# Performance work log

Hardware: AMD Instinct MI355X
Metric: run time of the kernel (lower is better)

Reference implementation:

```python
import math
import jax, jax.numpy as jnp
import numpy as np

B, L, D = 2, 2048, 2048
H, DH = 16, 128
DFF = 8192


def setup_inputs() -> dict:
    key = jax.random.key(0)
    ks = jax.random.split(key, 9)
    x = jax.random.normal(ks[0], (B, L, D), dtype=jnp.float32)
    # additive causal mask: 0 on/below diagonal, -inf above
    neg = jnp.finfo(jnp.float32).min
    mask = jnp.where(jnp.tril(jnp.ones((L, L), dtype=bool)), 0.0, neg)[None, None]
    s = 0.02
    return {
        "x": x,
        "mask": mask,
        "ln1_w": jnp.ones((D,), jnp.float32),
        "wq": jax.random.normal(ks[1], (D, D), jnp.float32) * s,
        "wk": jax.random.normal(ks[2], (D, D), jnp.float32) * s,
        "wv": jax.random.normal(ks[3], (D, D), jnp.float32) * s,
        "wo": jax.random.normal(ks[4], (D, D), jnp.float32) * s,
        "ln2_w": jnp.ones((D,), jnp.float32),
        "w_up": jax.random.normal(ks[5], (DFF, D), jnp.float32) * s,
        "w_down": jax.random.normal(ks[6], (D, DFF), jnp.float32) * s,
    }


def _rmsnorm(x, w, eps=1e-8):
    rms = jnp.sqrt(jnp.mean(x * x, axis=-1, keepdims=True) + eps)
    return x / rms * w


def reference(x, mask, ln1_w, wq, wk, wv, wo, ln2_w, w_up, w_down):
    h = _rmsnorm(x, ln1_w)
    # torch Linear: y = x @ W.T ; weights are [out, in]
    q = (h @ wq.T).reshape(B, L, H, DH).transpose(0, 2, 1, 3)  # [B,H,L,DH]
    k = (h @ wk.T).reshape(B, L, H, DH).transpose(0, 2, 1, 3)
    v = (h @ wv.T).reshape(B, L, H, DH).transpose(0, 2, 1, 3)
    scores = jnp.einsum('bhqd,bhkd->bhqk', q, k) / math.sqrt(DH)
    scores = scores + mask
    attn = jax.nn.softmax(scores, axis=-1)
    out = jnp.einsum('bhqk,bhkd->bhqd', attn, v)
    out = out.transpose(0, 2, 1, 3).reshape(B, L, D)
    x = x + out @ wo.T
    h = _rmsnorm(x, ln2_w)
    ff = jax.nn.gelu(h @ w_up.T, approximate=False) @ w_down.T  # exact erf GELU as in F.gelu
    return x + ff
```

## Files before the change

### kernel.cpp

```cpp
#include <hip/hip_runtime.h>
#include <hip/hip_bf16.h>
#include <math.h>

#define B_   2
#define L_   2048
#define D_   2048
#define H_   16
#define DH_  128
#define DFF_ 8192
#define NTOK (B_*L_)

typedef __attribute__((ext_vector_type(8))) short bf16x8;
typedef __attribute__((ext_vector_type(4))) float floatx4;
typedef unsigned short u16;

__device__ __forceinline__ u16 f2bf(float f) {
    union { float f; unsigned u; } c; c.f = f;
    unsigned r = (c.u + 0x7fffu + ((c.u >> 16) & 1u)) >> 16;
    return (u16)r;
}

__device__ __forceinline__ void async_cp16(const u16* g, u16* l) {
    __builtin_amdgcn_global_load_lds(
        (const __attribute__((address_space(1))) unsigned int*)g,
        (__attribute__((address_space(3))) unsigned int*)l,
        16, 0, 0);
}

__global__ __launch_bounds__(256) void cvt_bf16(const float* __restrict__ in,
                                                u16* __restrict__ out, int n4) {
    int i = blockIdx.x * 256 + threadIdx.x;
    if (i >= n4) return;
    float4 v = ((const float4*)in)[i];
    ushort4 o = { f2bf(v.x), f2bf(v.y), f2bf(v.z), f2bf(v.w) };
    ((ushort4*)out)[i] = o;
}

__global__ __launch_bounds__(256) void rmsnorm_kernel(const float* __restrict__ x,
                                                      const float* __restrict__ w,
                                                      u16* __restrict__ out) {
    const int row = blockIdx.x, tid = threadIdx.x;
    const float* xr = x + (size_t)row * D_;
    float4 a = ((const float4*)xr)[tid];
    float4 b = ((const float4*)xr)[tid + 256];
    float ss = a.x*a.x + a.y*a.y + a.z*a.z + a.w*a.w
             + b.x*b.x + b.y*b.y + b.z*b.z + b.w*b.w;
#pragma unroll
    for (int d = 1; d < 64; d <<= 1) ss += __shfl_xor(ss, d, 64);
    __shared__ float sred[4];
    if ((tid & 63) == 0) sred[tid >> 6] = ss;
    __syncthreads();
    float tot = sred[0] + sred[1] + sred[2] + sred[3];
    float inv = 1.0f / sqrtf(tot * (1.0f / D_) + 1e-8f);
    float4 w0 = ((const float4*)w)[tid];
    float4 w1 = ((const float4*)w)[tid + 256];
    ushort4 o0 = { f2bf(a.x*inv*w0.x), f2bf(a.y*inv*w0.y), f2bf(a.z*inv*w0.z), f2bf(a.w*inv*w0.w) };
    ushort4 o1 = { f2bf(b.x*inv*w1.x), f2bf(b.y*inv*w1.y), f2bf(b.z*inv*w1.z), f2bf(b.w*inv*w1.w) };
    ushort4* orow = (ushort4*)(out + (size_t)row * D_);
    orow[tid] = o0;
    orow[tid + 256] = o1;
}


template<int MODE>
__global__ __launch_bounds__(512, 2) void gemm256(const u16* __restrict__ A,
                                                  const u16* __restrict__ Bw,
                                                  void* __restrict__ outp,
                                                  void* __restrict__ outp2,
                                                  const float* __restrict__ residual,
                                                  int M, int N, int K, float scale) {
    __shared__ __attribute__((aligned(16))) u16 lds_a[2][256 * 64];
    __shared__ __attribute__((aligned(16))) u16 lds_b[2][256 * 64];
    const int tid = threadIdx.x;
    const int wave = tid >> 6, lane = tid & 63;
    const int qd = lane >> 4, c16 = lane & 15;
    const int wm = wave >> 2, wn = wave & 3;
    const int gx = gridDim.x;
    const int nwg = gx * gridDim.y;
    const int orig = blockIdx.y * gx + blockIdx.x;
    const int id2 = (orig & 7) * (nwg >> 3) + (orig >> 3);
    const long tile_m = (long)(id2 / gx) * 256, tile_n = (long)(id2 % gx) * 256;
    const int NT = K >> 6;

    const int srow = tid >> 3;
    const int scol = (((tid & 7) ^ (srow & 7))) * 8;
    const u16* Asrc = A + (tile_m + srow) * (long)K + scol;
    const u16* Bsrc = Bw + (tile_n + srow) * (long)K + scol;
    const int stoff = tid * 8;

#define STAGE_A2(bi, g0, g1, ko) do { \
        async_cp16(Asrc + (long)(g0) * 64 * K + (ko), &lds_a[bi][(g0) * 4096 + stoff]); \
        async_cp16(Asrc + (long)(g1) * 64 * K + (ko), &lds_a[bi][(g1) * 4096 + stoff]); \
    } while (0)
#define STAGE_B2(bi, g0, g1, ko) do { \
        async_cp16(Bsrc + (long)(g0) * 64 * K + (ko), &lds_b[bi][(g0) * 4096 + stoff]); \
        async_cp16(Bsrc + (long)(g1) * 64 * K + (ko), &lds_b[bi][(g1) * 4096 + stoff]); \
    } while (0)

    const int csw = (qd * 16) ^ ((c16 & 7) << 4);
    const int arowb = (wm * 128 + c16) * 128;
    const int browb = (wn * 64 + c16) * 128;
#define LDAF(bi, i, ks) (*(const bf16x8*)((const char*)&lds_a[bi][0] + arowb + (i) * 2048 + (csw ^ ((ks) * 64))))
#define LDBF(bi, j, ks) (*(const bf16x8*)((const char*)&lds_b[bi][0] + browb + (j) * 2048 + (csw ^ ((ks) * 64))))
#define MFMA_(a, b, c) __builtin_amdgcn_mfma_f32_16x16x32_bf16(a, b, c, 0, 0, 0)

#define READ_BFR(bi) do { \
        _Pragma("unroll") \
        for (int j = 0; j < 4; j++) { bfr[j][0] = LDBF(bi, j, 0); bfr[j][1] = LDBF(bi, j, 1); } \
    } while (0)
#define READ_AF(dst, bi, r0) do { \
        dst[0] = LDAF(bi, r0, 0); dst[1] = LDAF(bi, r0, 1); \
        dst[2] = LDAF(bi, (r0) + 1, 0); dst[3] = LDAF(bi, (r0) + 1, 1); \
    } while (0)
#define MFMA_PH(af, R) do { \
        __builtin_amdgcn_s_setprio(1); \
        _Pragma("unroll") \
        for (int j = 0; j < 4; j++) acc[R][j]       = MFMA_(af[0], bfr[j][0], acc[R][j]); \
        _Pragma("unroll") \
        for (int j = 0; j < 4; j++) acc[(R) + 1][j] = MFMA_(af[2], bfr[j][0], acc[(R) + 1][j]); \
        _Pragma("unroll") \
        for (int j = 0; j < 4; j++) acc[R][j]       = MFMA_(af[1], bfr[j][1], acc[R][j]); \
        _Pragma("unroll") \
        for (int j = 0; j < 4; j++) acc[(R) + 1][j] = MFMA_(af[3], bfr[j][1], acc[(R) + 1][j]); \
        __builtin_amdgcn_s_setprio(0); \
    } while (0)

    floatx4 acc[8][4] = {};
    bf16x8 bfr[4][2];

    STAGE_B2(0, 0, 1, 0); STAGE_B2(0, 2, 3, 0);
    STAGE_A2(0, 0, 2, 0); STAGE_A2(0, 1, 3, 0);
    STAGE_B2(1, 0, 1, 64); STAGE_B2(1, 2, 3, 64);
    STAGE_A2(1, 0, 2, 64);
    asm volatile("s_waitcnt vmcnt(6)" ::: "memory");
    __builtin_amdgcn_s_barrier();

#define TILE256(bi, koN, koNN, GA1, GS) do { \
        READ_BFR(bi); \
        bf16x8 afA[4], afB[4]; \
        READ_AF(afA, bi, 0); \
         \
        READ_AF(afB, bi, 2); \
        if (GA1) STAGE_A2((bi) ^ 1, 1, 3, koN); \
        MFMA_PH(afA, 0); \
        __builtin_amdgcn_s_barrier(); \
         \
        READ_AF(afA, bi, 4); \
        if (GS) STAGE_B2(bi, 0, 1, koNN); \
        MFMA_PH(afB, 2); \
        __builtin_amdgcn_s_barrier(); \
         \
        READ_AF(afB, bi, 6); \
        if (GS) STAGE_B2(bi, 2, 3, koNN); \
        MFMA_PH(afA, 4); \
        __builtin_amdgcn_s_barrier(); \
         \
        if (GS) STAGE_A2(bi, 0, 2, koNN); \
        MFMA_PH(afB, 6); \
        if (GS) asm volatile("s_waitcnt vmcnt(6)" ::: "memory"); \
        else    asm volatile("s_waitcnt vmcnt(0)" ::: "memory"); \
        __builtin_amdgcn_s_barrier(); \
    } while (0)

    for (int t = 0; t < NT; t += 2) {
        const int s2 = (t + 2) < NT;
        const long ko1 = (long)(t + 1) * 64;
        const long ko2 = (long)(t + 2) * 64;
        const long ko3 = (long)(t + 3) * 64;
        TILE256(0, ko1, ko2, 1, s2);
        TILE256(1, ko2, ko3, s2, s2);
    }

#pragma unroll
    for (int i = 0; i < 8; i++) {
#pragma unroll
        for (int j = 0; j < 4; j++) {
#pragma unroll
            for (int r = 0; r < 4; r++) {
                long m = tile_m + wm * 128 + i * 16 + qd * 4 + r;
                long n = tile_n + wn * 64 + j * 16 + c16;
                float v = acc[i][j][r];
                if (MODE == 0) {
                    long b = m >> 11, l = m & 2047;
                    int isq = n < D_;
                    long f = n & 2047, h = f >> 7, dh = f & 127;
                    u16* dst = isq ? (u16*)outp : (u16*)outp2;
                    dst[((b * H_ + h) * (long)L_ + l) * DH_ + dh] =
                        f2bf(v * (isq ? scale : 1.0f));
                } else if (MODE == 1) {
                    long idx = m * (long)N + n;
                    ((float*)outp)[idx] = v + residual[idx];
                } else if (MODE == 2) {
                    float g = 0.5f * v * (1.0f + erff(v * 0.70710678118654752f));
                    ((u16*)outp)[m * (long)N + n] = f2bf(g);
                } else {
                    ((u16*)outp)[m * (long)N + n] = f2bf(v);
                }
            }
        }
    }
#undef TILE256
#undef READ_BFR
#undef READ_AF
#undef MFMA_PH
#undef STAGE_A2
#undef STAGE_B2
#undef LDAF
#undef LDBF
#undef MFMA_
}

template<int MODE>
__global__ __launch_bounds__(512, 2) void gemm128n(const u16* __restrict__ A,
                                                   const u16* __restrict__ Bw,
                                                   void* __restrict__ outp,
                                                   const float* __restrict__ residual,
                                                   int M, int N, int K) {
    __shared__ __attribute__((aligned(16))) u16 lds_a[2][128 * 64];
    __shared__ __attribute__((aligned(16))) u16 lds_b[2][256 * 64];
    const int tid = threadIdx.x;
    const int wave = tid >> 6, lane = tid & 63;
    const int qd = lane >> 4, c16 = lane & 15;
    const int wm = wave >> 2, wn = wave & 3;
    const int gx = gridDim.x;
    const int nwg = gx * gridDim.y;
    const int orig = blockIdx.y * gx + blockIdx.x;
    const int id2 = (orig & 7) * (nwg >> 3) + (orig >> 3);
    const long tile_m = (long)(id2 / gx) * 128, tile_n = (long)(id2 % gx) * 256;
    const int NT = K >> 6;

    const int srow = tid >> 3;
    const int scol = (((tid & 7) ^ (srow & 7))) * 8;
    const u16* Asrc = A + (tile_m + srow) * (long)K + scol;
    const u16* Bsrc = Bw + (tile_n + srow) * (long)K + scol;
    const int stoff = tid * 8;

#define STAGE_AA(bi, ko) do { \
        async_cp16(Asrc + (ko), &lds_a[bi][stoff]); \
        async_cp16(Asrc + 64 * (long)K + (ko), &lds_a[bi][4096 + stoff]); \
    } while (0)
#define STAGE_BA(bi, ko) do { \
        async_cp16(Bsrc + (ko), &lds_b[bi][stoff]); \
        async_cp16(Bsrc + 64 * (long)K + (ko), &lds_b[bi][4096 + stoff]); \
        async_cp16(Bsrc + 128 * (long)K + (ko), &lds_b[bi][8192 + stoff]); \
        async_cp16(Bsrc + 192 * (long)K + (ko), &lds_b[bi][12288 + stoff]); \
    } while (0)

    const int csw = (qd * 16) ^ ((c16 & 7) << 4);
    const int arowb = (wm * 64 + c16) * 128;
    const int browb = (wn * 64 + c16) * 128;
#define LDAF2(bi, i, ks) (*(const bf16x8*)((const char*)&lds_a[bi][0] + arowb + (i) * 2048 + (csw ^ ((ks) * 64))))
#define LDBF2(bi, j, ks) (*(const bf16x8*)((const char*)&lds_b[bi][0] + browb + (j) * 2048 + (csw ^ ((ks) * 64))))
#define MFMA_(a, b, c) __builtin_amdgcn_mfma_f32_16x16x32_bf16(a, b, c, 0, 0, 0)

#define READ_BFR2(bi) do { \
        _Pragma("unroll") \
        for (int j = 0; j < 4; j++) { bfr[j][0] = LDBF2(bi, j, 0); bfr[j][1] = LDBF2(bi, j, 1); } \
    } while (0)
#define READ_AF2(dst, bi, r0) do { \
        dst[0] = LDAF2(bi, r0, 0); dst[1] = LDAF2(bi, r0, 1); \
        dst[2] = LDAF2(bi, (r0) + 1, 0); dst[3] = LDAF2(bi, (r0) + 1, 1); \
    } while (0)
#define MFMA_PH2(af, R) do { \
        __builtin_amdgcn_s_setprio(1); \
        _Pragma("unroll") \
        for (int j = 0; j < 4; j++) acc[R][j]       = MFMA_(af[0], bfr[j][0], acc[R][j]); \
        _Pragma("unroll") \
        for (int j = 0; j < 4; j++) acc[(R) + 1][j] = MFMA_(af[2], bfr[j][0], acc[(R) + 1][j]); \
        _Pragma("unroll") \
        for (int j = 0; j < 4; j++) acc[R][j]       = MFMA_(af[1], bfr[j][1], acc[R][j]); \
        _Pragma("unroll") \
        for (int j = 0; j < 4; j++) acc[(R) + 1][j] = MFMA_(af[3], bfr[j][1], acc[(R) + 1][j]); \
        __builtin_amdgcn_s_setprio(0); \
    } while (0)

    floatx4 acc[4][4] = {};
    bf16x8 bfr[4][2];

    STAGE_BA(0, 0); STAGE_AA(0, 0); STAGE_BA(1, 64);
    asm volatile("s_waitcnt vmcnt(4)" ::: "memory");
    __builtin_amdgcn_s_barrier();

#define TILE128(bi, koN, koNN, GA1, GS) do { \
        READ_BFR2(bi); \
        bf16x8 afA[4], afB[4]; \
        READ_AF2(afA, bi, 0); \
         \
        READ_AF2(afB, bi, 2); \
        if (GA1) STAGE_AA((bi) ^ 1, koN); \
        MFMA_PH2(afA, 0); \
        __builtin_amdgcn_s_barrier(); \
         \
        if (GS) STAGE_BA(bi, koNN); \
        MFMA_PH2(afB, 2); \
        if (GS) asm volatile("s_waitcnt vmcnt(4)" ::: "memory"); \
        else    asm volatile("s_waitcnt vmcnt(0)" ::: "memory"); \
        __builtin_amdgcn_s_barrier(); \
    } while (0)

    for (int t = 0; t < NT; t += 2) {
        const int g1 = (t + 1) < NT, s2 = (t + 2) < NT;
        const long ko1 = (long)(t + 1) * 64;
        const long ko2 = (long)(t + 2) * 64;
        const long ko3 = (long)(t + 3) * 64;
        TILE128(0, ko1, ko2, g1, s2);
        TILE128(1, ko2, ko3, s2, s2);
    }

#pragma unroll
    for (int i = 0; i < 4; i++) {
#pragma unroll
        for (int j = 0; j < 4; j++) {
#pragma unroll
            for (int r = 0; r < 4; r++) {
                long m = tile_m + wm * 64 + i * 16 + qd * 4 + r;
                long n = tile_n + wn * 64 + j * 16 + c16;
                float v = acc[i][j][r];
                if (MODE == 1) {
                    long idx = m * (long)N + n;
                    ((float*)outp)[idx] = v + residual[idx];
                } else {
                    ((u16*)outp)[m * (long)N + n] = f2bf(v);
                }
            }
        }
    }
#undef TILE128
#undef READ_BFR2
#undef READ_AF2
#undef MFMA_PH2
#undef STAGE_AA
#undef STAGE_BA
#undef LDAF2
#undef LDBF2
#undef MFMA_
}

#define KSTRIDE 136
#define VSTRIDE 72
#define PSTRIDE 72
__global__ __launch_bounds__(256) void attn_kernel(const u16* __restrict__ Q,
                                                   const u16* __restrict__ K,
                                                   const u16* __restrict__ VT,
                                                   u16* __restrict__ O) {
    __shared__ __attribute__((aligned(16))) u16 kt_lds[64 * KSTRIDE];
    __shared__ __attribute__((aligned(16))) u16 vt_lds[128 * VSTRIDE];
    __shared__ __attribute__((aligned(16))) u16 p_lds[4][16 * PSTRIDE];
    const int tid = threadIdx.x;
    const int wave = tid >> 6, lane = tid & 63;
    const int qd = lane >> 4, c16 = lane & 15;
    const int pair = blockIdx.x, bh = blockIdx.y;
    const int b = bh >> 4, h = bh & 15;
    const u16* qh = Q + (size_t)bh * L_ * DH_;
    const u16* kh = K + (size_t)bh * L_ * DH_;
    const u16* vth = VT + (size_t)h * DH_ * NTOK + (size_t)b * L_;

    for (int qsel = 0; qsel < 2; ++qsel) {
        const int qt = qsel ? (31 - pair) : pair;
        const int q0 = qt * 64;

        bf16x8 qf[4];
#pragma unroll
        for (int s = 0; s < 4; s++)
            qf[s] = *(const bf16x8*)(qh + (size_t)(q0 + wave * 16 + c16) * DH_ + s * 32 + qd * 8);

        floatx4 o_acc[8] = {};
        float m_i[4], l_i[4];
#pragma unroll
        for (int r = 0; r < 4; r++) { m_i[r] = -1e30f; l_i[r] = 0.f; }

        for (int kt = 0; kt <= qt; kt++) {
            const int kv0 = kt * 64;
#pragma unroll
            for (int s = 0; s < 4; s++) {
                int c = tid + s * 256;
                int kr = c >> 4, koff = (c & 15) * 8;
                *(int4*)&kt_lds[kr * KSTRIDE + koff] =
                    *(const int4*)(kh + (size_t)(kv0 + kr) * DH_ + koff);
                int dh = c >> 3, kv8 = (c & 7) * 8;
                *(int4*)&vt_lds[dh * VSTRIDE + kv8] =
                    *(const int4*)(vth + (size_t)dh * NTOK + kv0 + kv8);
            }
            __syncthreads();

            floatx4 s_acc[4] = {};
#pragma unroll
            for (int s = 0; s < 4; s++)
#pragma unroll
                for (int j = 0; j < 4; j++) {
                    bf16x8 kf = *(const bf16x8*)&kt_lds[(j * 16 + c16) * KSTRIDE + s * 32 + qd * 8];
                    s_acc[j] = __builtin_amdgcn_mfma_f32_16x16x32_bf16(qf[s], kf, s_acc[j], 0, 0, 0);
                }

            if (kt == qt) {
#pragma unroll
                for (int j = 0; j < 4; j++)
#pragma unroll
                    for (int r = 0; r < 4; r++) {
                        int col = j * 16 + c16;
                        int row = wave * 16 + qd * 4 + r;
                        if (col > row) s_acc[j][r] = -1e30f;
                    }
            }

            float rsum[4], alpha[4];
#pragma unroll
            for (int r = 0; r < 4; r++) {
                float mx = fmaxf(fmaxf(s_acc[0][r], s_acc[1][r]), fmaxf(s_acc[2][r], s_acc[3][r]));
#pragma unroll
                for (int d = 1; d < 16; d <<= 1) mx = fmaxf(mx, __shfl_xor(mx, d, 64));
                float mnew = fmaxf(m_i[r], mx);
                alpha[r] = __expf(m_i[r] - mnew);
                m_i[r] = mnew;
                rsum[r] = 0.f;
            }
#pragma unroll
            for (int j = 0; j < 4; j++)
#pragma unroll
                for (int r = 0; r < 4; r++) {
                    float p = __expf(s_acc[j][r] - m_i[r]);
                    s_acc[j][r] = p;
                    rsum[r] += p;
                }
#pragma unroll
            for (int r = 0; r < 4; r++) {
#pragma unroll
                for (int d = 1; d < 16; d <<= 1) rsum[r] += __shfl_xor(rsum[r], d, 64);
                l_i[r] = l_i[r] * alpha[r] + rsum[r];
            }
#pragma unroll
            for (int j8 = 0; j8 < 8; j8++)
#pragma unroll
                for (int r = 0; r < 4; r++) o_acc[j8][r] *= alpha[r];

#pragma unroll
            for (int j = 0; j < 4; j++)
#pragma unroll
                for (int r = 0; r < 4; r++)
                    p_lds[wave][(qd * 4 + r) * PSTRIDE + j * 16 + c16] = f2bf(s_acc[j][r]);

#pragma unroll
            for (int s = 0; s < 2; s++) {
                bf16x8 pf = *(const bf16x8*)&p_lds[wave][c16 * PSTRIDE + s * 32 + qd * 8];
#pragma unroll
                for (int j8 = 0; j8 < 8; j8++) {
                    bf16x8 vf = *(const bf16x8*)&vt_lds[(j8 * 16 + c16) * VSTRIDE + s * 32 + qd * 8];
                    o_acc[j8] = __builtin_amdgcn_mfma_f32_16x16x32_bf16(pf, vf, o_acc[j8], 0, 0, 0);
                }
            }
            __syncthreads();
        }

        float inv_l[4];
#pragma unroll
        for (int r = 0; r < 4; r++) inv_l[r] = 1.0f / l_i[r];
#pragma unroll
        for (int j8 = 0; j8 < 8; j8++)
#pragma unroll
            for (int r = 0; r < 4; r++) {
                int l = q0 + wave * 16 + qd * 4 + r;
                int d = h * DH_ + j8 * 16 + c16;
                O[(size_t)(b * L_ + l) * D_ + d] = f2bf(o_acc[j8][r] * inv_l[r]);
            }
    }
}

extern "C" void kernel_launch(void* const* d_in, const int* in_sizes, int n_in,
                              void* d_out, int out_size, void* d_ws, size_t ws_size,
                              hipStream_t stream) {
    const float* x     = (const float*)d_in[0];
    const float* ln1_w = (const float*)d_in[2];
    const float* wq    = (const float*)d_in[3];
    const float* wk    = (const float*)d_in[4];
    const float* wv    = (const float*)d_in[5];
    const float* wo    = (const float*)d_in[6];
    const float* ln2_w = (const float*)d_in[7];
    const float* w_up  = (const float*)d_in[8];
    const float* w_dn  = (const float*)d_in[9];

    char* ws = (char*)d_ws;
    const size_t MB = 1024 * 1024;
    float* x2   = (float*)(ws + 0);
    u16* hbuf   = (u16*)(ws + 32 * MB);
    u16* qbuf   = (u16*)(ws + 48 * MB);
    u16* kbuf   = (u16*)(ws + 64 * MB);
    u16* vtbuf  = (u16*)(ws + 80 * MB);
    u16* attnb  = (u16*)(ws + 96 * MB);
    u16* upbuf  = (u16*)(ws + 48 * MB);
    u16* wbufA  = (u16*)(ws + 112 * MB);
    u16* wbufC  = (u16*)(ws + 128 * MB);

    dim3 blk(256), blk512(512);
    const int nW = D_ * D_;
    const int nU = DFF_ * D_;
    cvt_bf16<<<(nW / 4 + 255) / 256, blk, 0, stream>>>(wq, wbufA, nW / 4);
    cvt_bf16<<<(nW / 4 + 255) / 256, blk, 0, stream>>>(wk, wbufA + (size_t)nW, nW / 4);
    cvt_bf16<<<(nW / 4 + 255) / 256, blk, 0, stream>>>(wv, wbufC, nW / 4);
    rmsnorm_kernel<<<NTOK, blk, 0, stream>>>(x, ln1_w, hbuf);

    gemm256<0><<<dim3(2 * D_ / 256, NTOK / 256), blk512, 0, stream>>>(
        hbuf, wbufA, qbuf, kbuf, nullptr, NTOK, 2 * D_, D_, 0.08838834764831845f);
    gemm128n<3><<<dim3(NTOK / 256, D_ / 128), blk512, 0, stream>>>(
        wbufC, hbuf, vtbuf, nullptr, D_, NTOK, D_);

    dim3 ga(16, B_ * H_);
    attn_kernel<<<ga, blk, 0, stream>>>(qbuf, kbuf, vtbuf, attnb);

    cvt_bf16<<<(nW / 4 + 255) / 256, blk, 0, stream>>>(wo, wbufA, nW / 4);
    gemm128n<1><<<dim3(D_ / 256, NTOK / 128), blk512, 0, stream>>>(
        attnb, wbufA, x2, x, NTOK, D_, D_);

    rmsnorm_kernel<<<NTOK, blk, 0, stream>>>(x2, ln2_w, hbuf);

    cvt_bf16<<<(nU / 4 + 255) / 256, blk, 0, stream>>>(w_up, wbufA, nU / 4);
    gemm256<2><<<dim3(DFF_ / 256, NTOK / 256), blk512, 0, stream>>>(
        hbuf, wbufA, upbuf, nullptr, nullptr, NTOK, DFF_, D_, 1.0f);

    cvt_bf16<<<(nU / 4 + 255) / 256, blk, 0, stream>>>(w_dn, wbufA, nU / 4);
    gemm128n<1><<<dim3(D_ / 256, NTOK / 128), blk512, 0, stream>>>(
        upbuf, wbufA, (float*)d_out, x2, NTOK, D_, DFF_);
}
```

Measured before the change: 782.7 us.

## Restructure GEMM main loop into barrier-separated load/MFMA phases

Reorganizes both GEMM kernels' inner tile loops into phases where each phase issues its LDS fragment reads and the next async global-to-LDS stage, waits on lgkmcnt, hits a barrier, then runs the MFMA block followed by another barrier. This replaces the previous software-pipelined scheme that prefetched the next phase's A fragments during the current MFMAs. The intent is a ping-pong schedule where waves alternate between memory and MFMA phases to reduce contention. It doubles the barriers per tile and removes register-level prefetch overlap, so LDS latency may be exposed.

```diff
diff --git a/kernel.cpp b/kernel.cpp
--- a/kernel.cpp
+++ b/kernel.cpp
@@ -104,27 +104,6 @@
 #define LDBF(bi, j, ks) (*(const bf16x8*)((const char*)&lds_b[bi][0] + browb + (j) * 2048 + (csw ^ ((ks) * 64))))
 #define MFMA_(a, b, c) __builtin_amdgcn_mfma_f32_16x16x32_bf16(a, b, c, 0, 0, 0)
 
-#define READ_BFR(bi) do { \
-        _Pragma("unroll") \
-        for (int j = 0; j < 4; j++) { bfr[j][0] = LDBF(bi, j, 0); bfr[j][1] = LDBF(bi, j, 1); } \
-    } while (0)
-#define READ_AF(dst, bi, r0) do { \
-        dst[0] = LDAF(bi, r0, 0); dst[1] = LDAF(bi, r0, 1); \
-        dst[2] = LDAF(bi, (r0) + 1, 0); dst[3] = LDAF(bi, (r0) + 1, 1); \
-    } while (0)
-#define MFMA_PH(af, R) do { \
-        __builtin_amdgcn_s_setprio(1); \
-        _Pragma("unroll") \
-        for (int j = 0; j < 4; j++) acc[R][j]       = MFMA_(af[0], bfr[j][0], acc[R][j]); \
-        _Pragma("unroll") \
-        for (int j = 0; j < 4; j++) acc[(R) + 1][j] = MFMA_(af[2], bfr[j][0], acc[(R) + 1][j]); \
-        _Pragma("unroll") \
-        for (int j = 0; j < 4; j++) acc[R][j]       = MFMA_(af[1], bfr[j][1], acc[R][j]); \
-        _Pragma("unroll") \
-        for (int j = 0; j < 4; j++) acc[(R) + 1][j] = MFMA_(af[3], bfr[j][1], acc[(R) + 1][j]); \
-        __builtin_amdgcn_s_setprio(0); \
-    } while (0)
-
     floatx4 acc[8][4] = {};
     bf16x8 bfr[4][2];
 
@@ -135,31 +114,39 @@
     asm volatile("s_waitcnt vmcnt(6)" ::: "memory");
     __builtin_amdgcn_s_barrier();
 
+#define PH256(bi, p, STAGE, PREW) do { \
+        if ((p) == 0) { \
+            _Pragma("unroll") \
+            for (int j = 0; j < 4; j++) { bfr[j][0] = LDBF(bi, j, 0); bfr[j][1] = LDBF(bi, j, 1); } \
+        } \
+        bf16x8 af[4]; \
+        af[0] = LDAF(bi, 2 * (p), 0);     af[1] = LDAF(bi, 2 * (p), 1); \
+        af[2] = LDAF(bi, 2 * (p) + 1, 0); af[3] = LDAF(bi, 2 * (p) + 1, 1); \
+        STAGE \
+        if ((p) == 0) asm volatile("s_waitcnt lgkmcnt(8)" ::: "memory"); \
+        PREW \
+        __builtin_amdgcn_s_barrier(); \
+        asm volatile("s_waitcnt lgkmcnt(0)" ::: "memory"); \
+        __builtin_amdgcn_s_setprio(1); \
+        _Pragma("unroll") \
+        for (int j = 0; j < 4; j++) acc[2 * (p)][j]     = MFMA_(af[0], bfr[j][0], acc[2 * (p)][j]); \
+        _Pragma("unroll") \
+        for (int j = 0; j < 4; j++) acc[2 * (p) + 1][j] = MFMA_(af[2], bfr[j][0], acc[2 * (p) + 1][j]); \
+        _Pragma("unroll") \
+        for (int j = 0; j < 4; j++) acc[2 * (p)][j]     = MFMA_(af[1], bfr[j][1], acc[2 * (p)][j]); \
+        _Pragma("unroll") \
+        for (int j = 0; j < 4; j++) acc[2 * (p) + 1][j] = MFMA_(af[3], bfr[j][1], acc[2 * (p) + 1][j]); \
+        __builtin_amdgcn_s_setprio(0); \
+        __builtin_amdgcn_s_barrier(); \
+    } while (0)
+
 #define TILE256(bi, koN, koNN, GA1, GS) do { \
-        READ_BFR(bi); \
-        bf16x8 afA[4], afB[4]; \
-        READ_AF(afA, bi, 0); \
-         \
-        READ_AF(afB, bi, 2); \
-        if (GA1) STAGE_A2((bi) ^ 1, 1, 3, koN); \
-        MFMA_PH(afA, 0); \
-        __builtin_amdgcn_s_barrier(); \
-         \
-        READ_AF(afA, bi, 4); \
-        if (GS) STAGE_B2(bi, 0, 1, koNN); \
-        MFMA_PH(afB, 2); \
-        __builtin_amdgcn_s_barrier(); \
-         \
-        READ_AF(afB, bi, 6); \
-        if (GS) STAGE_B2(bi, 2, 3, koNN); \
-        MFMA_PH(afA, 4); \
-        __builtin_amdgcn_s_barrier(); \
-         \
-        if (GS) STAGE_A2(bi, 0, 2, koNN); \
-        MFMA_PH(afB, 6); \
-        if (GS) asm volatile("s_waitcnt vmcnt(6)" ::: "memory"); \
-        else    asm volatile("s_waitcnt vmcnt(0)" ::: "memory"); \
-        __builtin_amdgcn_s_barrier(); \
+        PH256(bi, 0, if (GA1) STAGE_A2((bi) ^ 1, 1, 3, koN);, ); \
+        PH256(bi, 1, if (GS) STAGE_B2(bi, 0, 1, koNN);, ); \
+        PH256(bi, 2, if (GS) STAGE_B2(bi, 2, 3, koNN);, ); \
+        PH256(bi, 3, if (GS) STAGE_A2(bi, 0, 2, koNN);, \
+              if (GS) asm volatile("s_waitcnt vmcnt(6)" ::: "memory"); \
+              else    asm volatile("s_waitcnt vmcnt(0)" ::: "memory");); \
     } while (0)
 
     for (int t = 0; t < NT; t += 2) {
@@ -200,9 +187,7 @@
         }
     }
 #undef TILE256
-#undef READ_BFR
-#undef READ_AF
-#undef MFMA_PH
+#undef PH256
 #undef STAGE_A2
 #undef STAGE_B2
 #undef LDAF
@@ -253,27 +238,6 @@
 #define LDBF2(bi, j, ks) (*(const bf16x8*)((const char*)&lds_b[bi][0] + browb + (j) * 2048 + (csw ^ ((ks) * 64))))
 #define MFMA_(a, b, c) __builtin_amdgcn_mfma_f32_16x16x32_bf16(a, b, c, 0, 0, 0)
 
-#define READ_BFR2(bi) do { \
-        _Pragma("unroll") \
-        for (int j = 0; j < 4; j++) { bfr[j][0] = LDBF2(bi, j, 0); bfr[j][1] = LDBF2(bi, j, 1); } \
-    } while (0)
-#define READ_AF2(dst, bi, r0) do { \
-        dst[0] = LDAF2(bi, r0, 0); dst[1] = LDAF2(bi, r0, 1); \
-        dst[2] = LDAF2(bi, (r0) + 1, 0); dst[3] = LDAF2(bi, (r0) + 1, 1); \
-    } while (0)
-#define MFMA_PH2(af, R) do { \
-        __builtin_amdgcn_s_setprio(1); \
-        _Pragma("unroll") \
-        for (int j = 0; j < 4; j++) acc[R][j]       = MFMA_(af[0], bfr[j][0], acc[R][j]); \
-        _Pragma("unroll") \
-        for (int j = 0; j < 4; j++) acc[(R) + 1][j] = MFMA_(af[2], bfr[j][0], acc[(R) + 1][j]); \
-        _Pragma("unroll") \
-        for (int j = 0; j < 4; j++) acc[R][j]       = MFMA_(af[1], bfr[j][1], acc[R][j]); \
-        _Pragma("unroll") \
-        for (int j = 0; j < 4; j++) acc[(R) + 1][j] = MFMA_(af[3], bfr[j][1], acc[(R) + 1][j]); \
-        __builtin_amdgcn_s_setprio(0); \
-    } while (0)
-
     floatx4 acc[4][4] = {};
     bf16x8 bfr[4][2];
 
@@ -281,21 +245,37 @@
     asm volatile("s_waitcnt vmcnt(4)" ::: "memory");
     __builtin_amdgcn_s_barrier();
 
+#define PH128(bi, p, STAGE, PREW) do { \
+        if ((p) == 0) { \
+            _Pragma("unroll") \
+            for (int j = 0; j < 4; j++) { bfr[j][0] = LDBF2(bi, j, 0); bfr[j][1] = LDBF2(bi, j, 1); } \
+        } \
+        bf16x8 af[4]; \
+        af[0] = LDAF2(bi, 2 * (p), 0);     af[1] = LDAF2(bi, 2 * (p), 1); \
+        af[2] = LDAF2(bi, 2 * (p) + 1, 0); af[3] = LDAF2(bi, 2 * (p) + 1, 1); \
+        STAGE \
+        if ((p) == 0) asm volatile("s_waitcnt lgkmcnt(8)" ::: "memory"); \
+        PREW \
+        __builtin_amdgcn_s_barrier(); \
+        asm volatile("s_waitcnt lgkmcnt(0)" ::: "memory"); \
+        __builtin_amdgcn_s_setprio(1); \
+        _Pragma("unroll") \
+        for (int j = 0; j < 4; j++) acc[2 * (p)][j]     = MFMA_(af[0], bfr[j][0], acc[2 * (p)][j]); \
+        _Pragma("unroll") \
+        for (int j = 0; j < 4; j++) acc[2 * (p) + 1][j] = MFMA_(af[2], bfr[j][0], acc[2 * (p) + 1][j]); \
+        _Pragma("unroll") \
+        for (int j = 0; j < 4; j++) acc[2 * (p)][j]     = MFMA_(af[1], bfr[j][1], acc[2 * (p)][j]); \
+        _Pragma("unroll") \
+        for (int j = 0; j < 4; j++) acc[2 * (p) + 1][j] = MFMA_(af[3], bfr[j][1], acc[2 * (p) + 1][j]); \
+        __builtin_amdgcn_s_setprio(0); \
+        __builtin_amdgcn_s_barrier(); \
+    } while (0)
+
 #define TILE128(bi, koN, koNN, GA1, GS) do { \
-        READ_BFR2(bi); \
-        bf16x8 afA[4], afB[4]; \
-        READ_AF2(afA, bi, 0); \
-         \
-        READ_AF2(afB, bi, 2); \
-        if (GA1) STAGE_AA((bi) ^ 1, koN); \
-        MFMA_PH2(afA, 0); \
-        __builtin_amdgcn_s_barrier(); \
-         \
-        if (GS) STAGE_BA(bi, koNN); \
-        MFMA_PH2(afB, 2); \
-        if (GS) asm volatile("s_waitcnt vmcnt(4)" ::: "memory"); \
-        else    asm volatile("s_waitcnt vmcnt(0)" ::: "memory"); \
-        __builtin_amdgcn_s_barrier(); \
+        PH128(bi, 0, if (GA1) STAGE_AA((bi) ^ 1, koN);, ); \
+        PH128(bi, 1, if (GS) STAGE_BA(bi, koNN);, \
+              if (GS) asm volatile("s_waitcnt vmcnt(4)" ::: "memory"); \
+              else    asm volatile("s_waitcnt vmcnt(0)" ::: "memory");); \
     } while (0)
 
     for (int t = 0; t < NT; t += 2) {
@@ -326,9 +306,7 @@
         }
     }
 #undef TILE128
-#undef READ_BFR2
-#undef READ_AF2
-#undef MFMA_PH2
+#undef PH128
 #undef STAGE_AA
 #undef STAGE_BA
 #undef LDAF2
```

New measurement: 795.6 us. No clear change (+1.6%).
